# Performance work log

Measured on AMD Instinct MI355X. Metric: run time of the kernel, lower is better.

The kernel has to match this reference:

```python
import jax, jax.numpy as jnp
import numpy as np

BATCH, LENGTH, DIM = 8, 65536, 128
MAX_N_PEAKS = 512


def setup_inputs() -> dict:
    rng = np.random.default_rng(0)
    # per-sample number of peaks (each sample also has one trailing dropped chunk)
    n_peaks = rng.integers(400, MAX_N_PEAKS + 1, size=BATCH)
    chunk_sizes = []
    for i in range(BATCH):
        # n_peaks[i] cut points -> n_peaks[i]+1 chunks summing exactly to LENGTH
        cuts = np.sort(rng.choice(np.arange(1, LENGTH), size=int(n_peaks[i]), replace=False))
        sizes = np.diff(np.concatenate([[0], cuts, [LENGTH]]))
        chunk_sizes.append(sizes)
    chunk_size = np.concatenate(chunk_sizes).astype(np.int32)
    key = jax.random.key(0)
    x = jax.random.normal(key, (BATCH, LENGTH, DIM), dtype=jnp.float32)
    return {
        "x": x,
        "chunk_size": jnp.asarray(chunk_size),
        "n_peaks": jnp.asarray(n_peaks, dtype=jnp.int32),
        "max_n_peaks": MAX_N_PEAKS,
    }


def reference(x, chunk_size, n_peaks, max_n_peaks):
    # x: (B, L, D); chunk_size: (total_chunks,) summing to B*L;
    # n_peaks: (B,); sample i owns chunks [pool_start[i], pool_start[i]+n_peaks[i]+1),
    # the last chunk of each sample is dropped (matches pool_end = pool_idx - 1).
    batch, length, dim = x.shape
    total_chunks = chunk_size.shape[0]  # static
    x_flat = x.reshape(-1, dim)  # (B*L, D)

    # one fused segment-mean over all chunks
    seg_ids = jnp.repeat(jnp.arange(total_chunks), chunk_size,
                         total_repeat_length=batch * length)
    sums = jax.ops.segment_sum(x_flat, seg_ids, num_segments=total_chunks)
    counts = jnp.maximum(chunk_size, 1).astype(x.dtype)  # empty chunk -> zeros
    means = sums / counts[:, None]  # (total_chunks, D)

    # map chunk -> (sample, peak slot), scatter into padded output
    chunks_per_sample = n_peaks + 1
    pool_start = jnp.concatenate(
        [jnp.zeros((1,), n_peaks.dtype), jnp.cumsum(chunks_per_sample)[:-1]])
    sample_of_chunk = jnp.repeat(jnp.arange(batch), chunks_per_sample,
                                 total_repeat_length=total_chunks)
    peak_pos = jnp.arange(total_chunks) - pool_start[sample_of_chunk]
    valid = peak_pos < n_peaks[sample_of_chunk]  # drops trailing chunk per sample
    dest = jnp.where(valid, peak_pos, max_n_peaks)  # invalid -> scratch row
    out = jnp.zeros((batch, max_n_peaks + 1, dim), x.dtype)
    out = out.at[sample_of_chunk, dest].set(means)
    return out[:, :max_n_peaks]  # (B, max_n_peaks, D), zero-padded
```

## Files before the change

### kernel.cpp

```cpp
#include <hip/hip_runtime.h>
#include <hip/hip_bf16.h>


#define SCAN_THREADS 256
#define TILE_ROWS 128

#define SCAN_BLOCKS 64
__global__ __launch_bounds__(SCAN_THREADS) void scan_zero_kernel(
    const int* __restrict__ chunk_size, const int* __restrict__ n_peaks,
    int total_chunks, int batch,
    int* __restrict__ chunk_start, int* __restrict__ pool_start,
    float4* __restrict__ sums) {
  const int nf4 = total_chunks * 32;
  for (int idx = blockIdx.x * SCAN_THREADS + threadIdx.x; idx < nf4;
       idx += SCAN_BLOCKS * SCAN_THREADS) {
    sums[idx] = make_float4(0.f, 0.f, 0.f, 0.f);
  }
  if (blockIdx.x != 0) return;

  __shared__ int partials[SCAN_THREADS];
  const int t = threadIdx.x;
  const int items = (total_chunks + SCAN_THREADS - 1) / SCAN_THREADS;
  const int begin = t * items;
  const int end = min(begin + items, total_chunks);

  int local = 0;
  for (int i = begin; i < end; ++i) local += chunk_size[i];
  partials[t] = local;
  __syncthreads();

  for (int off = 1; off < SCAN_THREADS; off <<= 1) {
    int v = (t >= off) ? partials[t - off] : 0;
    __syncthreads();
    partials[t] += v;
    __syncthreads();
  }

  int run = (t == 0) ? 0 : partials[t - 1];
  for (int i = begin; i < end; ++i) {
    chunk_start[i] = run;
    run += chunk_size[i];
  }

  if (t == 0) {
    int acc = 0;
    for (int i = 0; i < batch; ++i) {
      pool_start[i] = acc;
      acc += n_peaks[i] + 1;
    }
  }
}

__global__ __launch_bounds__(256) void tile_sum_kernel(
    const float* __restrict__ x, const int* __restrict__ chunk_start,
    float* __restrict__ sums, int total_chunks, int total_rows) {
  const int t = threadIdx.x;
  const int dim4 = t & 31;
  const int r0 = t >> 5;
  const int tile_begin = blockIdx.x * TILE_ROWS;
  const int tile_end = min(tile_begin + TILE_ROWS, total_rows);

  int lo = 0, hi = total_chunks - 1;
  while (lo < hi) {
    int mid = (lo + hi + 1) >> 1;
    if (chunk_start[mid] <= tile_begin) lo = mid; else hi = mid - 1;
  }
  int c = lo;

  const float4* __restrict__ xp = (const float4*)x;
  __shared__ float4 red[256];

  int seg_begin = tile_begin;
  while (seg_begin < tile_end) {
    const int chunk_end = (c + 1 < total_chunks) ? chunk_start[c + 1] : total_rows;
    const int seg_end = min(chunk_end, tile_end);

    float4 acc = make_float4(0.f, 0.f, 0.f, 0.f);
#pragma unroll 4
    for (int r = seg_begin + r0; r < seg_end; r += 8) {
      float4 v = xp[(size_t)r * 32 + dim4];
      acc.x += v.x; acc.y += v.y; acc.z += v.z; acc.w += v.w;
    }

    red[t] = acc;
    __syncthreads();
    if (t < 32) {
      float4 s = red[t];
#pragma unroll
      for (int k = 1; k < 8; ++k) {
        float4 v = red[t + 32 * k];
        s.x += v.x; s.y += v.y; s.z += v.z; s.w += v.w;
      }
      float* dst = sums + (size_t)c * 128 + t * 4;
      atomicAdd(dst + 0, s.x);
      atomicAdd(dst + 1, s.y);
      atomicAdd(dst + 2, s.z);
      atomicAdd(dst + 3, s.w);
    }
    __syncthreads();
    seg_begin = seg_end;
    ++c;
  }
}

__global__ __launch_bounds__(256) void combine_kernel(
    const float4* __restrict__ sums, const int* __restrict__ chunk_size,
    const int* __restrict__ n_peaks, const int* __restrict__ pool_start,
    float4* __restrict__ out, int max_n_peaks, int n_slots) {
  const int t = threadIdx.x;
  const int slot = blockIdx.x * 8 + (t >> 5);
  const int dim4 = t & 31;
  if (slot >= n_slots) return;
  const int i = slot / max_n_peaks;
  const int p = slot % max_n_peaks;

  float4 m = make_float4(0.f, 0.f, 0.f, 0.f);
  if (p < n_peaks[i]) {
    const int c = pool_start[i] + p;
    float4 s = sums[(size_t)c * 32 + dim4];
    const int sz = chunk_size[c];
    const float inv = 1.0f / (float)(sz > 0 ? sz : 1);
    m = make_float4(s.x * inv, s.y * inv, s.z * inv, s.w * inv);
  }
  out[(size_t)slot * 32 + dim4] = m;
}

extern "C" void kernel_launch(void* const* d_in, const int* in_sizes, int n_in,
                              void* d_out, int out_size, void* d_ws, size_t ws_size,
                              hipStream_t stream) {
  const float* x = (const float*)d_in[0];
  const int* chunk_size = (const int*)d_in[1];
  const int* n_peaks = (const int*)d_in[2];
  const int total_chunks = in_sizes[1];
  const int batch = in_sizes[2];
  const int dim = 128;
  const int max_n_peaks = out_size / (batch * dim);
  const int total_rows = in_sizes[0] / dim;
  float* out = (float*)d_out;

  int* chunk_start = (int*)d_ws;
  int* pool_start = chunk_start + total_chunks;
  size_t off = ((size_t)(total_chunks + batch) * sizeof(int) + 15) & ~(size_t)15;
  float* sums = (float*)((char*)d_ws + off);

  scan_zero_kernel<<<SCAN_BLOCKS, SCAN_THREADS, 0, stream>>>(
      chunk_size, n_peaks, total_chunks, batch, chunk_start, pool_start,
      (float4*)sums);

  const int n_tiles = (total_rows + TILE_ROWS - 1) / TILE_ROWS;
  tile_sum_kernel<<<n_tiles, 256, 0, stream>>>(x, chunk_start, sums,
                                               total_chunks, total_rows);

  const int n_slots = batch * max_n_peaks;
  combine_kernel<<<(n_slots + 7) / 8, 256, 0, stream>>>(
      (const float4*)sums, chunk_size, n_peaks, pool_start, (float4*)out,
      max_n_peaks, n_slots);
}
```

Baseline: 374.2 us.

## Fuse mean and scatter into tile-sum kernel, drop combine pass

```diff
diff --git a/kernel.cpp b/kernel.cpp
--- a/kernel.cpp
+++ b/kernel.cpp
@@ -3,18 +3,17 @@
 
 
 #define SCAN_THREADS 256
-#define TILE_ROWS 128
+#define SCAN_BLOCKS 64
+#define TILE_ROWS 256
 
-#define SCAN_BLOCKS 64
-__global__ __launch_bounds__(SCAN_THREADS) void scan_zero_kernel(
+__global__ __launch_bounds__(SCAN_THREADS) void scan_zero_out_kernel(
     const int* __restrict__ chunk_size, const int* __restrict__ n_peaks,
-    int total_chunks, int batch,
+    int total_chunks, int batch, int total_rows,
     int* __restrict__ chunk_start, int* __restrict__ pool_start,
-    float4* __restrict__ sums) {
-  const int nf4 = total_chunks * 32;
-  for (int idx = blockIdx.x * SCAN_THREADS + threadIdx.x; idx < nf4;
+    float4* __restrict__ out, int out_f4) {
+  for (int idx = blockIdx.x * SCAN_THREADS + threadIdx.x; idx < out_f4;
        idx += SCAN_BLOCKS * SCAN_THREADS) {
-    sums[idx] = make_float4(0.f, 0.f, 0.f, 0.f);
+    out[idx] = make_float4(0.f, 0.f, 0.f, 0.f);
   }
   if (blockIdx.x != 0) return;
 
@@ -43,17 +42,21 @@
   }
 
   if (t == 0) {
+    chunk_start[total_chunks] = total_rows;
     int acc = 0;
     for (int i = 0; i < batch; ++i) {
       pool_start[i] = acc;
       acc += n_peaks[i] + 1;
     }
+    pool_start[batch] = acc;
   }
 }
 
-__global__ __launch_bounds__(256) void tile_sum_kernel(
+__global__ __launch_bounds__(256, 8) void tile_sum_scatter_kernel(
     const float* __restrict__ x, const int* __restrict__ chunk_start,
-    float* __restrict__ sums, int total_chunks, int total_rows) {
+    const int* __restrict__ pool_start, const int* __restrict__ n_peaks,
+    float* __restrict__ out, int total_chunks, int total_rows, int batch,
+    int max_n_peaks) {
   const int t = threadIdx.x;
   const int dim4 = t & 31;
   const int r0 = t >> 5;
@@ -66,14 +69,17 @@
     if (chunk_start[mid] <= tile_begin) lo = mid; else hi = mid - 1;
   }
   int c = lo;
+  int samp = 0;
+  while (pool_start[samp + 1] <= c) ++samp;
 
   const float4* __restrict__ xp = (const float4*)x;
   __shared__ float4 red[256];
 
   int seg_begin = tile_begin;
+  int c_begin = chunk_start[c];
   while (seg_begin < tile_end) {
-    const int chunk_end = (c + 1 < total_chunks) ? chunk_start[c + 1] : total_rows;
-    const int seg_end = min(chunk_end, tile_end);
+    const int c_end = chunk_start[c + 1];
+    const int seg_end = min(c_end, tile_end);
 
     float4 acc = make_float4(0.f, 0.f, 0.f, 0.f);
 #pragma unroll 4
@@ -84,45 +90,31 @@
 
     red[t] = acc;
     __syncthreads();
-    if (t < 32) {
+
+    const int peak = c - pool_start[samp];
+    const bool valid = peak < n_peaks[samp];
+    if (valid && t < 32) {
       float4 s = red[t];
 #pragma unroll
       for (int k = 1; k < 8; ++k) {
         float4 v = red[t + 32 * k];
         s.x += v.x; s.y += v.y; s.z += v.z; s.w += v.w;
       }
-      float* dst = sums + (size_t)c * 128 + t * 4;
-      atomicAdd(dst + 0, s.x);
-      atomicAdd(dst + 1, s.y);
-      atomicAdd(dst + 2, s.z);
-      atomicAdd(dst + 3, s.w);
+      const int sz = c_end - c_begin;
+      const float inv = 1.0f / (float)(sz > 0 ? sz : 1);
+      float* dst = out + ((size_t)samp * max_n_peaks + peak) * 128 + t * 4;
+      atomicAdd(dst + 0, s.x * inv);
+      atomicAdd(dst + 1, s.y * inv);
+      atomicAdd(dst + 2, s.z * inv);
+      atomicAdd(dst + 3, s.w * inv);
     }
     __syncthreads();
+
     seg_begin = seg_end;
     ++c;
+    c_begin = c_end;
+    if (pool_start[samp + 1] <= c) ++samp;
   }
-}
-
-__global__ __launch_bounds__(256) void combine_kernel(
-    const float4* __restrict__ sums, const int* __restrict__ chunk_size,
-    const int* __restrict__ n_peaks, const int* __restrict__ pool_start,
-    float4* __restrict__ out, int max_n_peaks, int n_slots) {
-  const int t = threadIdx.x;
-  const int slot = blockIdx.x * 8 + (t >> 5);
-  const int dim4 = t & 31;
-  if (slot >= n_slots) return;
-  const int i = slot / max_n_peaks;
-  const int p = slot % max_n_peaks;
-
-  float4 m = make_float4(0.f, 0.f, 0.f, 0.f);
-  if (p < n_peaks[i]) {
-    const int c = pool_start[i] + p;
-    float4 s = sums[(size_t)c * 32 + dim4];
-    const int sz = chunk_size[c];
-    const float inv = 1.0f / (float)(sz > 0 ? sz : 1);
-    m = make_float4(s.x * inv, s.y * inv, s.z * inv, s.w * inv);
-  }
-  out[(size_t)slot * 32 + dim4] = m;
 }
 
 extern "C" void kernel_launch(void* const* d_in, const int* in_sizes, int n_in,
@@ -139,20 +131,14 @@
   float* out = (float*)d_out;
 
   int* chunk_start = (int*)d_ws;
-  int* pool_start = chunk_start + total_chunks;
-  size_t off = ((size_t)(total_chunks + batch) * sizeof(int) + 15) & ~(size_t)15;
-  float* sums = (float*)((char*)d_ws + off);
+  int* pool_start = chunk_start + (total_chunks + 1);
 
-  scan_zero_kernel<<<SCAN_BLOCKS, SCAN_THREADS, 0, stream>>>(
-      chunk_size, n_peaks, total_chunks, batch, chunk_start, pool_start,
-      (float4*)sums);
+  scan_zero_out_kernel<<<SCAN_BLOCKS, SCAN_THREADS, 0, stream>>>(
+      chunk_size, n_peaks, total_chunks, batch, total_rows, chunk_start,
+      pool_start, (float4*)out, out_size / 4);
 
   const int n_tiles = (total_rows + TILE_ROWS - 1) / TILE_ROWS;
-  tile_sum_kernel<<<n_tiles, 256, 0, stream>>>(x, chunk_start, sums,
-                                               total_chunks, total_rows);
-
-  const int n_slots = batch * max_n_peaks;
-  combine_kernel<<<(n_slots + 7) / 8, 256, 0, stream>>>(
-      (const float4*)sums, chunk_size, n_peaks, pool_start, (float4*)out,
-      max_n_peaks, n_slots);
+  tile_sum_scatter_kernel<<<n_tiles, 256, 0, stream>>>(
+      x, chunk_start, pool_start, n_peaks, out, total_chunks, total_rows,
+      batch, max_n_peaks);
 }
```

New measurement: 373.6 us. No clear change (-0.2%).
